# Performance work log

Measured on AMD Instinct MI355X. Metric: run time of the kernel, lower is better.

The kernel has to match this reference:

```python
import jax, jax.numpy as jnp
import numpy as np

B, DIM, H, W = 2, 192, 64, 64
HEADS = 4
EPS = 1e-12  # torch F.normalize eps


def conv2d(x, w, groups=1):
    # x: NCHW, w: OIHW, stride 1, SAME padding
    return jax.lax.conv_general_dilated(
        x, w, window_strides=(1, 1), padding='SAME',
        feature_group_count=groups,
        dimension_numbers=('NCHW', 'OIHW', 'NCHW'))


def setup_inputs() -> dict:
    key = jax.random.key(0)
    k1, k2, k3, k4 = jax.random.split(key, 4)
    x = jax.random.normal(k1, (B, DIM, H, W), dtype=jnp.float32)
    qkv_w = jax.random.normal(k2, (3 * DIM, DIM, 1, 1), dtype=jnp.float32) * 0.05
    dw_w = jax.random.normal(k3, (3 * DIM, 1, 3, 3), dtype=jnp.float32) * 0.05
    proj_w = jax.random.normal(k4, (DIM, DIM, 1, 1), dtype=jnp.float32) * 0.05
    temperature = jnp.ones((HEADS, 1, 1), dtype=jnp.float32)
    return {'x': x, 'qkv_w': qkv_w, 'dw_w': dw_w, 'proj_w': proj_w,
            'temperature': temperature}


def reference(x, qkv_w, dw_w, proj_w, temperature):
    b, dim, h, w = x.shape
    heads = temperature.shape[0]
    c = dim // heads  # per-head channels

    qkv = conv2d(conv2d(x, qkv_w), dw_w, groups=3 * dim)  # [b, 3*dim, h, w]
    q, k, v = jnp.split(qkv, 3, axis=1)

    def to_heads(t):
        # b (head c) h w -> b head (h w) c
        return t.reshape(b, heads, c, h * w).transpose(0, 1, 3, 2)

    q, k, v = to_heads(q), to_heads(k), to_heads(v)

    def l2norm(t):
        n = jnp.linalg.norm(t, axis=-1, keepdims=True)
        return t / jnp.maximum(n, EPS)

    q = l2norm(q)
    k = l2norm(k)

    # cosine attention with per-head learnable temperature
    attn = jnp.einsum('bnqc,bnkc->bnqk', q, k) * temperature[None]
    attn = jax.nn.softmax(attn, axis=-1)
    out = jnp.einsum('bnqk,bnkc->bnqc', attn, v)  # [b, head, hw, c]

    # b head (h w) c -> b (head c) h w
    out = out.transpose(0, 1, 3, 2).reshape(b, dim, h, w)
    return conv2d(out, proj_w)
```

## Files before the change

### kernel.cpp

```cpp
#include <hip/hip_runtime.h>
#include <cstdint>
#include <cstddef>

#define HW    4096
#define IMG   64
#define DIMC  192
#define NH    4
#define CH    48
#define CPAD  64
#define KVSPLIT 4
#define NTILE (HW / 64 / KVSPLIT)
#define LOG2E 1.4426950408889634f

typedef __bf16 bf16x8 __attribute__((ext_vector_type(8)));
typedef float  f32x4  __attribute__((ext_vector_type(4)));
typedef unsigned short u16x8 __attribute__((ext_vector_type(8)));

#if __has_builtin(__builtin_amdgcn_exp2f)
#define EXP2(x) __builtin_amdgcn_exp2f(x)
#else
#define EXP2(x) exp2f(x)
#endif

__device__ __forceinline__ unsigned short f2bf(float f) {
  unsigned int u = __builtin_bit_cast(unsigned int, f);
  u = (u + 0x7FFFu + ((u >> 16) & 1u)) >> 16;
  return (unsigned short)u;
}
__device__ __forceinline__ float bf2f(unsigned short u) {
  return __builtin_bit_cast(float, (unsigned int)u << 16);
}
__device__ __forceinline__ f32x4 mfma16(bf16x8 a, bf16x8 b, f32x4 c) {
  return __builtin_amdgcn_mfma_f32_16x16x32_bf16(a, b, c, 0, 0, 0);
}
__device__ __forceinline__ void gl16(const void* g, void* l) {
  __builtin_amdgcn_global_load_lds(
      (const __attribute__((address_space(1))) unsigned int*)g,
      (__attribute__((address_space(3))) unsigned int*)l, 16, 0, 0);
}

__global__ __launch_bounds__(256) void pack2_kernel(
    const float* __restrict__ x, const float* __restrict__ qkv_w,
    const float* __restrict__ proj_w, unsigned short* __restrict__ xb,
    unsigned short* __restrict__ wqkv, unsigned short* __restrict__ wproj) {
  const int bx = blockIdx.x, tid = threadIdx.x;
  if (bx < 64) {
    const int half = bx & 1;
    const int gpx = (bx >> 1) * 256 + tid;
    const int b = gpx >> 12, p = gpx & 4095;
    const int ch0 = half * 96;
    const float* src = x + ((size_t)b * DIMC + ch0) * HW + p;
    #pragma unroll
    for (int kc2 = 0; kc2 < 3; ++kc2) {
      const int kc = half * 3 + kc2;
      u16x8 g[4];
      #pragma unroll
      for (int v = 0; v < 4; ++v)
        #pragma unroll
        for (int j = 0; j < 8; ++j)
          g[v][j] = f2bf(src[(size_t)(kc2 * 32 + v * 8 + j) * HW]);
      unsigned short* dst = xb + (((size_t)b * 6 + kc) * HW + p) * 32;
      #pragma unroll
      for (int v = 0; v < 4; ++v) *(u16x8*)(dst + v * 8) = g[v];
    }
  } else {
    const int row = (bx - 64) * 256 + tid;
    if (row < 576) {
      const float* src = qkv_w + (size_t)row * DIMC;
      #pragma unroll
      for (int kc = 0; kc < 6; ++kc) {
        u16x8 g0, g1, g2, g3;
        #pragma unroll
        for (int j = 0; j < 8; ++j) {
          g0[j] = f2bf(src[kc * 32 + j]);      g1[j] = f2bf(src[kc * 32 + 8 + j]);
          g2[j] = f2bf(src[kc * 32 + 16 + j]); g3[j] = f2bf(src[kc * 32 + 24 + j]);
        }
        unsigned short* dst = wqkv + ((size_t)kc * 576 + row) * 32;
        *(u16x8*)dst = g0; *(u16x8*)(dst + 8) = g1;
        *(u16x8*)(dst + 16) = g2; *(u16x8*)(dst + 24) = g3;
      }
    } else {
      const int oc = row - 576;
      const float* src = proj_w + (size_t)oc * DIMC;
      #pragma unroll
      for (int kc = 0; kc < 6; ++kc) {
        u16x8 g0, g1, g2, g3;
        #pragma unroll
        for (int j = 0; j < 8; ++j) {
          g0[j] = f2bf(src[kc * 32 + j]);      g1[j] = f2bf(src[kc * 32 + 8 + j]);
          g2[j] = f2bf(src[kc * 32 + 16 + j]); g3[j] = f2bf(src[kc * 32 + 24 + j]);
        }
        unsigned short* dst = wproj + ((size_t)kc * DIMC + oc) * 32;
        *(u16x8*)dst = g0; *(u16x8*)(dst + 8) = g1;
        *(u16x8*)(dst + 16) = g2; *(u16x8*)(dst + 24) = g3;
      }
    }
  }
}

template <int PF, bool OBF>
__global__ __launch_bounds__(256) void wx_gemm2_kernel(
    const unsigned short* __restrict__ xb, const unsigned short* __restrict__ wb,
    void* __restrict__ Cout, int OC) {
  const int tid = threadIdx.x;
  const int lane = tid & 63, wv = tid >> 6;
  const int l15 = lane & 15, l4 = lane >> 4;
  const int oc0 = blockIdx.x * 64 + wv * 16;
  const int px0 = blockIdx.y * (PF * 16);
  const int b   = blockIdx.z;

  f32x4 acc[PF];
  #pragma unroll
  for (int p = 0; p < PF; ++p) acc[p] = f32x4{0.f, 0.f, 0.f, 0.f};

  #pragma unroll
  for (int kc = 0; kc < 6; ++kc) {
    const bf16x8 af = *(const bf16x8*)(wb + ((size_t)kc * OC + oc0 + l15) * 32 + l4 * 8);
    const unsigned short* xrow = xb + (((size_t)b * 6 + kc) * HW + px0 + l15) * 32 + l4 * 8;
    #pragma unroll
    for (int p = 0; p < PF; ++p) {
      const bf16x8 bf = *(const bf16x8*)(xrow + p * 512);
      acc[p] = mfma16(af, bf, acc[p]);
    }
  }
  if (OBF) {
    unsigned short* Cb = (unsigned short*)Cout + ((size_t)b * OC + oc0) * HW + px0;
    #pragma unroll
    for (int p = 0; p < PF; ++p)
      #pragma unroll
      for (int r = 0; r < 4; ++r)
        Cb[(size_t)(l4 * 4 + r) * HW + p * 16 + l15] = f2bf(acc[p][r]);
  } else {
    float* Cb = (float*)Cout + ((size_t)b * OC + oc0) * HW + px0;
    #pragma unroll
    for (int p = 0; p < PF; ++p)
      #pragma unroll
      for (int r = 0; r < 4; ++r)
        Cb[(size_t)(l4 * 4 + r) * HW + p * 16 + l15] = acc[p][r];
  }
}

__global__ __launch_bounds__(256) void dw_conv3_kernel(
    const unsigned short* __restrict__ X, const float* __restrict__ W,
    unsigned short* __restrict__ Y) {
  __shared__ float T[66][72];
  const int bc = blockIdx.x;
  const int ch = bc % 576;
  const int tid = threadIdx.x;
  const unsigned short* Xb = X + (size_t)bc * HW;
  #pragma unroll
  for (int i = 0; i < 4; ++i) {
    const int idx = i * 256 + tid;
    const int row = idx >> 4, c4 = (idx & 15) << 2;
    const ushort4 u = *(const ushort4*)(Xb + row * 64 + c4);
    float4 f; f.x = bf2f(u.x); f.y = bf2f(u.y); f.z = bf2f(u.z); f.w = bf2f(u.w);
    *(float4*)&T[row + 1][c4 + 4] = f;
  }
  if (tid < 72) { T[0][tid] = 0.f; T[65][tid] = 0.f; }
  if (tid >= 128 && tid < 194) { const int r = tid - 128; T[r][3] = 0.f; T[r][68] = 0.f; }
  float w[9];
  #pragma unroll
  for (int i = 0; i < 9; ++i) w[i] = W[ch * 9 + i];
  __syncthreads();

  const int xx = tid & 63, ys = (tid >> 6) << 4;
  const int c = xx + 4;
  float a0 = T[ys][c - 1],     a1 = T[ys][c],     a2 = T[ys][c + 1];
  float b0 = T[ys + 1][c - 1], b1 = T[ys + 1][c], b2 = T[ys + 1][c + 1];
  unsigned short* Yb = Y + (size_t)bc * HW;
  #pragma unroll
  for (int k = 0; k < 16; ++k) {
    const float c0 = T[ys + k + 2][c - 1], c1 = T[ys + k + 2][c], c2 = T[ys + k + 2][c + 1];
    const float s = w[0] * a0 + w[1] * a1 + w[2] * a2
                  + w[3] * b0 + w[4] * b1 + w[5] * b2
                  + w[6] * c0 + w[7] * c1 + w[8] * c2;
    Yb[(ys + k) * 64 + xx] = f2bf(s);
    a0 = b0; a1 = b1; a2 = b2; b0 = c0; b1 = c1; b2 = c2;
  }
}

__global__ __launch_bounds__(256) void norm_pack3_kernel(
    const unsigned short* __restrict__ Dw, const float* __restrict__ temp,
    unsigned short* __restrict__ Qr, unsigned short* __restrict__ Kr,
    unsigned short* __restrict__ Vs) {
  const int px = blockIdx.x * 256 + threadIdx.x;
  const int sel = blockIdx.y >> 2, h = blockIdx.y & 3;
  const int b = blockIdx.z;
  const int bh = b * NH + h;
  const unsigned short* base = Dw + ((size_t)b * 576 + sel * DIMC + h * CH) * HW + px;

  float v[CH];
  if (sel == 2) {
    const int kt = px & ~63, kl = px & 63;
    #pragma unroll
    for (int c = 0; c < CH; ++c)
      Vs[((size_t)bh * CH + c) * HW + kt + (kl ^ ((c & 7) << 3))] = base[(size_t)c * HW];
    return;
  }
  float ss = 0.f;
  #pragma unroll
  for (int j = 0; j < CH; ++j) { v[j] = bf2f(base[(size_t)j * HW]); ss += v[j] * v[j]; }
  const u16x8 zz = {0, 0, 0, 0, 0, 0, 0, 0};
  if (sel == 0) {
    const float sc = temp[h] * LOG2E / fmaxf(sqrtf(ss), 1e-12f);
    u16x8 gr[8];
    #pragma unroll
    for (int g = 0; g < 6; ++g)
      #pragma unroll
      for (int j = 0; j < 8; ++j) gr[g][j] = f2bf(v[g * 8 + j] * sc);
    gr[6] = zz; gr[7] = zz;
    unsigned short* qrow = Qr + ((size_t)bh * HW + px) * CPAD;
    #pragma unroll
    for (int g = 0; g < 8; ++g) *(u16x8*)(qrow + g * 8) = gr[g];
  } else {
    const int ksw = (px & 3) | (((px >> 3) & 1) << 2);
    const float sc = 1.0f / fmaxf(sqrtf(ss), 1e-12f);
    u16x8 gr[8];
    #pragma unroll
    for (int g = 0; g < 6; ++g)
      #pragma unroll
      for (int j = 0; j < 8; ++j) gr[g][j] = f2bf(v[g * 8 + j] * sc);
    gr[6] = zz; gr[7] = zz;
    unsigned short* krow = Kr + ((size_t)bh * HW + px) * CPAD;
    #pragma unroll
    for (int g = 0; g < 8; ++g) *(u16x8*)(krow + (g ^ ksw) * 8) = gr[g];
  }
}

__global__ __launch_bounds__(256, 2) void flash6_kernel(
    const unsigned short* __restrict__ Qr,
    const unsigned short* __restrict__ Kr,
    const unsigned short* __restrict__ Vs,
    const float* __restrict__ temp,
    unsigned short* __restrict__ Opart, float* __restrict__ Lpart) {
  __shared__ __align__(16) unsigned short Kl[2][64 * 64];
  __shared__ __align__(16) unsigned short Vl[2][64 * 64];
  const int tid = threadIdx.x;
  const int lane = tid & 63, wv = tid >> 6;
  const int l15 = lane & 15, l4 = lane >> 4;
  const int bh = blockIdx.x, qt = blockIdx.y, sp = blockIdx.z;
  const int qb = qt * 256 + wv * 64;
  const float m = fabsf(temp[bh & 3]) * LOG2E * 1.05f + 0.1f;

  for (int i = tid; i < 1024; i += 256) {
    const unsigned short vv = (i < 64) ? (unsigned short)0x3F80 : (unsigned short)0;
    Vl[0][3072 + i] = vv;
    Vl[1][3072 + i] = vv;
  }

  const unsigned short* Qb = Qr + ((size_t)bh * HW + qb) * CPAD;
  bf16x8 qf[4][2];
  #pragma unroll
  for (int qg = 0; qg < 4; ++qg)
    #pragma unroll
    for (int hh = 0; hh < 2; ++hh)
      qf[qg][hh] = *(const bf16x8*)(Qb + (size_t)(qg * 16 + l15) * CPAD + hh * 32 + l4 * 8);

  const char* kg = (const char*)Kr + ((size_t)bh * HW + (size_t)sp * (HW / KVSPLIT)) * 128;
  const char* vg = (const char*)Vs + (size_t)bh * CH * HW * 2 + (size_t)sp * (HW / KVSPLIT) * 2;
  const int koA = tid * 16;
  const int vgA = (tid >> 3) * 8192 + (tid & 7) * 16;
  const int vgB = (32 + (tid >> 3)) * 8192 + (tid & 7) * 16;

  auto stage = [&](int buf, const char* kp, const char* vp) {
    char* kl = (char*)&Kl[buf][0];
    gl16(kp + koA,        kl + koA);
    gl16(kp + 4096 + koA, kl + 4096 + koA);
    char* vl = (char*)&Vl[buf][0];
    gl16(vp + vgA, vl + tid * 16);
    if (tid < 128) gl16(vp + vgB, vl + 4096 + tid * 16);
  };

  f32x4 o[4][4];
  #pragma unroll
  for (int cg = 0; cg < 4; ++cg)
    #pragma unroll
    for (int qg = 0; qg < 4; ++qg) o[cg][qg] = f32x4{0.f, 0.f, 0.f, 0.f};
  const f32x4 zinit = {-m, -m, -m, -m};

  stage(0, kg, vg);
  kg += 8192; vg += 128;
  __syncthreads();
  int cur = 0;
  for (int t = 0; t < NTILE; ++t) {
    if (t + 1 < NTILE) { stage(cur ^ 1, kg, vg); kg += 8192; vg += 128; }
    const char* KL = (const char*)&Kl[cur][0];
    const char* VL = (const char*)&Vl[cur][0];

    f32x4 s[4][4];
    __builtin_amdgcn_s_setprio(1);
    #pragma unroll
    for (int n = 0; n < 4; ++n) {
      const int row = (n >> 1) * 32 + (l15 >> 2) * 8 + (n & 1) * 4 + (l15 & 3);
      const int sw = (l15 & 7) << 4;
      const bf16x8 kf0 = *(const bf16x8*)(KL + row * 128 + ((l4 << 4) ^ sw));
      const bf16x8 kf1 = *(const bf16x8*)(KL + row * 128 + (((4 + l4) << 4) ^ sw));
      #pragma unroll
      for (int qg = 0; qg < 4; ++qg) {
        f32x4 z = mfma16(kf0, qf[qg][0], zinit);
        s[qg][n] = mfma16(kf1, qf[qg][1], z);
      }
    }
    __builtin_amdgcn_s_setprio(0);

    #pragma unroll
    for (int qg = 0; qg < 4; ++qg)
      #pragma unroll
      for (int n = 0; n < 4; ++n)
        #pragma unroll
        for (int r = 0; r < 4; ++r)
          s[qg][n][r] = EXP2(s[qg][n][r]);

    #pragma unroll
    for (int kc = 0; kc < 2; ++kc) {
      bf16x8 pb[4];
      #pragma unroll
      for (int qg = 0; qg < 4; ++qg)
        #pragma unroll
        for (int j = 0; j < 8; ++j)
          pb[qg][j] = (__bf16)s[qg][kc * 2 + (j >> 2)][j & 3];
      __builtin_amdgcn_s_setprio(1);
      #pragma unroll
      for (int cg = 0; cg < 4; ++cg) {
        const int vrow = cg * 16 + l15;
        const bf16x8 vf = *(const bf16x8*)(VL + vrow * 128 + (((kc * 4 + l4) ^ (l15 & 7)) << 4));
        #pragma unroll
        for (int qg = 0; qg < 4; ++qg) o[cg][qg] = mfma16(vf, pb[qg], o[cg][qg]);
      }
      __builtin_amdgcn_s_setprio(0);
    }
    __syncthreads();
    cur ^= 1;
  }

  unsigned short* Ob = Opart + (size_t)(sp * 8 + bh) * CH * HW;
  #pragma unroll
  for (int cg = 0; cg < 3; ++cg)
    #pragma unroll
    for (int qg = 0; qg < 4; ++qg)
      #pragma unroll
      for (int r = 0; r < 4; ++r)
        Ob[(size_t)(cg * 16 + l4 * 4 + r) * HW + qb + qg * 16 + l15] = f2bf(o[cg][qg][r]);
  if (l4 == 0) {
    #pragma unroll
    for (int qg = 0; qg < 4; ++qg)
      Lpart[(size_t)(sp * 8 + bh) * HW + qb + qg * 16 + l15] = o[3][qg][0];
  }
}

__global__ __launch_bounds__(256) void combine3_kernel(
    const unsigned short* __restrict__ Opart, const float* __restrict__ Lpart,
    unsigned short* __restrict__ attnb) {
  const int tid = threadIdx.x;
  const int bh = blockIdx.x >> 5;
  const int q  = ((blockIdx.x & 31) << 7) + (tid & 127);
  const int half = tid >> 7;
  float lsum = 0.f;
  #pragma unroll
  for (int sp = 0; sp < KVSPLIT; ++sp) lsum += Lpart[(size_t)(sp * 8 + bh) * HW + q];
  const float inv = 1.f / lsum;
  const int b = bh >> 2, h = bh & 3;
  const int c0 = half * 24;
  float v[24];
  #pragma unroll
  for (int c = 0; c < 24; ++c) {
    float s = 0.f;
    #pragma unroll
    for (int sp = 0; sp < KVSPLIT; ++sp)
      s += bf2f(Opart[((size_t)(sp * 8 + bh) * CH + c0 + c) * HW + q]);
    v[c] = s * inv;
  }
  #pragma unroll
  for (int g = 0; g < 3; ++g) {
    const int ch0 = h * CH + c0 + g * 8;
    const int kc = ch0 >> 5, off = ch0 & 31;
    unsigned short* dst = attnb + (((size_t)b * 6 + kc) * HW + q) * 32 + off;
    u16x8 gg;
    #pragma unroll
    for (int j = 0; j < 8; ++j) gg[j] = f2bf(v[g * 8 + j]);
    *(u16x8*)dst = gg;
  }
}

extern "C" void kernel_launch(void* const* d_in, const int* in_sizes, int n_in,
                              void* d_out, int out_size, void* d_ws, size_t ws_size,
                              hipStream_t stream) {
  const float* x      = (const float*)d_in[0];
  const float* qkv_w  = (const float*)d_in[1];
  const float* dw_w   = (const float*)d_in[2];
  const float* proj_w = (const float*)d_in[3];
  const float* temp   = (const float*)d_in[4];

  char* ws = (char*)d_ws;
  unsigned short* xb    = (unsigned short*)(ws);
  unsigned short* wqkv  = (unsigned short*)(ws + 3145728);
  unsigned short* wproj = (unsigned short*)(ws + 3366912);
  unsigned short* qkvb  = (unsigned short*)(ws + 3440640);
  unsigned short* dwb   = (unsigned short*)(ws + 12877824);
  unsigned short* Qr    = (unsigned short*)(ws + 22315008);
  unsigned short* Kr    = (unsigned short*)(ws + 26509312);
  unsigned short* Vs    = (unsigned short*)(ws + 30703616);
  unsigned short* Opart = (unsigned short*)(ws + 33849344);
  float*          Lpart = (float*)(ws + 46432256);
  unsigned short* attnb = (unsigned short*)(ws + 46956544);

  pack2_kernel<<<dim3(67), 256, 0, stream>>>(x, qkv_w, proj_w, xb, wqkv, wproj);
  wx_gemm2_kernel<4, true><<<dim3(9, 64, 2), 256, 0, stream>>>(xb, wqkv, qkvb, 576);
  dw_conv3_kernel<<<dim3(1152), 256, 0, stream>>>(qkvb, dw_w, dwb);
  norm_pack3_kernel<<<dim3(16, 12, 2), 256, 0, stream>>>(dwb, temp, Qr, Kr, Vs);
  flash6_kernel<<<dim3(8, 16, KVSPLIT), 256, 0, stream>>>(Qr, Kr, Vs, temp, Opart, Lpart);
  combine3_kernel<<<dim3(256), 256, 0, stream>>>(Opart, Lpart, attnb);
  wx_gemm2_kernel<2, false><<<dim3(3, 128, 2), 256, 0, stream>>>(attnb, wproj, (float*)d_out, 192);
}
```

Measured before the change: 83.83 us.

## Use 32x32 MFMA in flash attention, fuse combine into projection GEMM

The attention kernel moves from 16x16x32 to 32x32x16 bf16 MFMA tiles and converts P to bf16 with packed converts plus a permlane32 swap. Its epilogue now goes through an LDS transpose so each query's output row is written contiguously. The split-KV combine kernel is removed and folded into the projection GEMM, which reduces the partials and normalises them while building its B operand. The QKV GEMM now reuses each activation fragment across three output-channel slices. Together these cut one launch and an intermediate buffer round trip, at the cost of fewer, heavier blocks in the GEMMs and more LDS and register pressure.

```diff
diff --git a/kernel.cpp b/kernel.cpp
--- a/kernel.cpp
+++ b/kernel.cpp
@@ -14,7 +14,9 @@
 
 typedef __bf16 bf16x8 __attribute__((ext_vector_type(8)));
 typedef float  f32x4  __attribute__((ext_vector_type(4)));
+typedef float  f32x16 __attribute__((ext_vector_type(16)));
 typedef unsigned short u16x8 __attribute__((ext_vector_type(8)));
+typedef unsigned int   u32x4 __attribute__((ext_vector_type(4)));
 
 #if __has_builtin(__builtin_amdgcn_exp2f)
 #define EXP2(x) __builtin_amdgcn_exp2f(x)
@@ -33,10 +35,21 @@
 __device__ __forceinline__ f32x4 mfma16(bf16x8 a, bf16x8 b, f32x4 c) {
   return __builtin_amdgcn_mfma_f32_16x16x32_bf16(a, b, c, 0, 0, 0);
 }
+__device__ __forceinline__ f32x16 mfma32(bf16x8 a, bf16x8 b, f32x16 c) {
+  return __builtin_amdgcn_mfma_f32_32x32x16_bf16(a, b, c, 0, 0, 0);
+}
 __device__ __forceinline__ void gl16(const void* g, void* l) {
   __builtin_amdgcn_global_load_lds(
       (const __attribute__((address_space(1))) unsigned int*)g,
       (__attribute__((address_space(3))) unsigned int*)l, 16, 0, 0);
+}
+__device__ __forceinline__ unsigned int cvtpk(float lo, float hi) {
+  unsigned int d;
+  asm("v_cvt_pk_bf16_f32 %0, %1, %2" : "=v"(d) : "v"(lo), "v"(hi));
+  return d;
+}
+__device__ __forceinline__ void swap32(unsigned int& a, unsigned int& b) {
+  asm("v_permlane32_swap_b32 %0, %1" : "+v"(a), "+v"(b));
 }
 
 __global__ __launch_bounds__(256) void pack2_kernel(
@@ -98,45 +111,44 @@
   }
 }
 
-template <int PF, bool OBF>
-__global__ __launch_bounds__(256) void wx_gemm2_kernel(
+__global__ __launch_bounds__(256) void qkv_gemm_kernel(
     const unsigned short* __restrict__ xb, const unsigned short* __restrict__ wb,
-    void* __restrict__ Cout, int OC) {
+    unsigned short* __restrict__ Cout) {
   const int tid = threadIdx.x;
   const int lane = tid & 63, wv = tid >> 6;
   const int l15 = lane & 15, l4 = lane >> 4;
-  const int oc0 = blockIdx.x * 64 + wv * 16;
-  const int px0 = blockIdx.y * (PF * 16);
+  const int ocbase = blockIdx.x * 192;
+  const int px0 = blockIdx.y * 64;
   const int b   = blockIdx.z;
 
-  f32x4 acc[PF];
-  #pragma unroll
-  for (int p = 0; p < PF; ++p) acc[p] = f32x4{0.f, 0.f, 0.f, 0.f};
+  f32x4 acc[3][4];
+  #pragma unroll
+  for (int s = 0; s < 3; ++s)
+    #pragma unroll
+    for (int p = 0; p < 4; ++p) acc[s][p] = f32x4{0.f, 0.f, 0.f, 0.f};
 
   #pragma unroll
   for (int kc = 0; kc < 6; ++kc) {
-    const bf16x8 af = *(const bf16x8*)(wb + ((size_t)kc * OC + oc0 + l15) * 32 + l4 * 8);
     const unsigned short* xrow = xb + (((size_t)b * 6 + kc) * HW + px0 + l15) * 32 + l4 * 8;
-    #pragma unroll
-    for (int p = 0; p < PF; ++p) {
-      const bf16x8 bf = *(const bf16x8*)(xrow + p * 512);
-      acc[p] = mfma16(af, bf, acc[p]);
-    }
-  }
-  if (OBF) {
-    unsigned short* Cb = (unsigned short*)Cout + ((size_t)b * OC + oc0) * HW + px0;
-    #pragma unroll
-    for (int p = 0; p < PF; ++p)
+    bf16x8 Bf[4];
+    #pragma unroll
+    for (int p = 0; p < 4; ++p) Bf[p] = *(const bf16x8*)(xrow + p * 512);
+    #pragma unroll
+    for (int s = 0; s < 3; ++s) {
+      const int oc = ocbase + s * 64 + wv * 16 + l15;
+      const bf16x8 af = *(const bf16x8*)(wb + ((size_t)kc * 576 + oc) * 32 + l4 * 8);
+      #pragma unroll
+      for (int p = 0; p < 4; ++p) acc[s][p] = mfma16(af, Bf[p], acc[s][p]);
+    }
+  }
+  #pragma unroll
+  for (int s = 0; s < 3; ++s) {
+    unsigned short* Cb = Cout + ((size_t)b * 576 + ocbase + s * 64 + wv * 16) * HW + px0;
+    #pragma unroll
+    for (int p = 0; p < 4; ++p)
       #pragma unroll
       for (int r = 0; r < 4; ++r)
-        Cb[(size_t)(l4 * 4 + r) * HW + p * 16 + l15] = f2bf(acc[p][r]);
-  } else {
-    float* Cb = (float*)Cout + ((size_t)b * OC + oc0) * HW + px0;
-    #pragma unroll
-    for (int p = 0; p < PF; ++p)
-      #pragma unroll
-      for (int r = 0; r < 4; ++r)
-        Cb[(size_t)(l4 * 4 + r) * HW + p * 16 + l15] = acc[p][r];
+        Cb[(size_t)(l4 * 4 + r) * HW + p * 16 + l15] = f2bf(acc[s][p][r]);
   }
 }
 
@@ -227,34 +239,36 @@
   }
 }
 
-__global__ __launch_bounds__(256, 2) void flash6_kernel(
+__global__ __launch_bounds__(256, 2) void flash7_kernel(
     const unsigned short* __restrict__ Qr,
     const unsigned short* __restrict__ Kr,
     const unsigned short* __restrict__ Vs,
     const float* __restrict__ temp,
     unsigned short* __restrict__ Opart, float* __restrict__ Lpart) {
-  __shared__ __align__(16) unsigned short Kl[2][64 * 64];
-  __shared__ __align__(16) unsigned short Vl[2][64 * 64];
+  __shared__ __align__(16) union {
+    struct { unsigned short Kl[2][4096]; unsigned short Vl[2][4096]; } s;
+    float T[256][53];
+  } lds;
   const int tid = threadIdx.x;
   const int lane = tid & 63, wv = tid >> 6;
-  const int l15 = lane & 15, l4 = lane >> 4;
+  const int l31 = lane & 31, lhi = lane >> 5;
   const int bh = blockIdx.x, qt = blockIdx.y, sp = blockIdx.z;
   const int qb = qt * 256 + wv * 64;
   const float m = fabsf(temp[bh & 3]) * LOG2E * 1.05f + 0.1f;
 
   for (int i = tid; i < 1024; i += 256) {
     const unsigned short vv = (i < 64) ? (unsigned short)0x3F80 : (unsigned short)0;
-    Vl[0][3072 + i] = vv;
-    Vl[1][3072 + i] = vv;
+    lds.s.Vl[0][3072 + i] = vv;
+    lds.s.Vl[1][3072 + i] = vv;
   }
 
   const unsigned short* Qb = Qr + ((size_t)bh * HW + qb) * CPAD;
-  bf16x8 qf[4][2];
-  #pragma unroll
-  for (int qg = 0; qg < 4; ++qg)
-    #pragma unroll
-    for (int hh = 0; hh < 2; ++hh)
-      qf[qg][hh] = *(const bf16x8*)(Qb + (size_t)(qg * 16 + l15) * CPAD + hh * 32 + l4 * 8);
+  bf16x8 qf[2][3];
+  #pragma unroll
+  for (int qb2 = 0; qb2 < 2; ++qb2)
+    #pragma unroll
+    for (int ci = 0; ci < 3; ++ci)
+      qf[qb2][ci] = *(const bf16x8*)(Qb + (size_t)(qb2 * 32 + l31) * CPAD + ci * 16 + lhi * 8);
 
   const char* kg = (const char*)Kr + ((size_t)bh * HW + (size_t)sp * (HW / KVSPLIT)) * 128;
   const char* vg = (const char*)Vs + (size_t)bh * CH * HW * 2 + (size_t)sp * (HW / KVSPLIT) * 2;
@@ -263,20 +277,24 @@
   const int vgB = (32 + (tid >> 3)) * 8192 + (tid & 7) * 16;
 
   auto stage = [&](int buf, const char* kp, const char* vp) {
-    char* kl = (char*)&Kl[buf][0];
+    char* kl = (char*)&lds.s.Kl[buf][0];
     gl16(kp + koA,        kl + koA);
     gl16(kp + 4096 + koA, kl + 4096 + koA);
-    char* vl = (char*)&Vl[buf][0];
+    char* vl = (char*)&lds.s.Vl[buf][0];
     gl16(vp + vgA, vl + tid * 16);
     if (tid < 128) gl16(vp + vgB, vl + 4096 + tid * 16);
   };
 
-  f32x4 o[4][4];
-  #pragma unroll
-  for (int cg = 0; cg < 4; ++cg)
-    #pragma unroll
-    for (int qg = 0; qg < 4; ++qg) o[cg][qg] = f32x4{0.f, 0.f, 0.f, 0.f};
-  const f32x4 zinit = {-m, -m, -m, -m};
+  f32x16 o[2][2];
+  #pragma unroll
+  for (int cb = 0; cb < 2; ++cb)
+    #pragma unroll
+    for (int qb2 = 0; qb2 < 2; ++qb2)
+      #pragma unroll
+      for (int i = 0; i < 16; ++i) o[cb][qb2][i] = 0.f;
+  f32x16 zin;
+  #pragma unroll
+  for (int i = 0; i < 16; ++i) zin[i] = -m;
 
   stage(0, kg, vg);
   kg += 8192; vg += 128;
@@ -284,48 +302,58 @@
   int cur = 0;
   for (int t = 0; t < NTILE; ++t) {
     if (t + 1 < NTILE) { stage(cur ^ 1, kg, vg); kg += 8192; vg += 128; }
-    const char* KL = (const char*)&Kl[cur][0];
-    const char* VL = (const char*)&Vl[cur][0];
-
-    f32x4 s[4][4];
+    const unsigned short* KL = &lds.s.Kl[cur][0];
+    const unsigned short* VL = &lds.s.Vl[cur][0];
+
+    f32x16 S[2][2];
     __builtin_amdgcn_s_setprio(1);
     #pragma unroll
-    for (int n = 0; n < 4; ++n) {
-      const int row = (n >> 1) * 32 + (l15 >> 2) * 8 + (n & 1) * 4 + (l15 & 3);
-      const int sw = (l15 & 7) << 4;
-      const bf16x8 kf0 = *(const bf16x8*)(KL + row * 128 + ((l4 << 4) ^ sw));
-      const bf16x8 kf1 = *(const bf16x8*)(KL + row * 128 + (((4 + l4) << 4) ^ sw));
-      #pragma unroll
-      for (int qg = 0; qg < 4; ++qg) {
-        f32x4 z = mfma16(kf0, qf[qg][0], zinit);
-        s[qg][n] = mfma16(kf1, qf[qg][1], z);
+    for (int kb = 0; kb < 2; ++kb) {
+      const int krow = kb * 32 + l31;
+      const int ksw = (krow & 3) | (((krow >> 3) & 1) << 2);
+      bf16x8 kf[3];
+      #pragma unroll
+      for (int ci = 0; ci < 3; ++ci)
+        kf[ci] = *(const bf16x8*)(KL + krow * 64 + (((ci * 2 + lhi) ^ ksw) * 8));
+      #pragma unroll
+      for (int qb2 = 0; qb2 < 2; ++qb2) {
+        f32x16 acc = zin;
+        #pragma unroll
+        for (int ci = 0; ci < 3; ++ci) acc = mfma32(kf[ci], qf[qb2][ci], acc);
+        S[kb][qb2] = acc;
       }
     }
     __builtin_amdgcn_s_setprio(0);
 
     #pragma unroll
-    for (int qg = 0; qg < 4; ++qg)
-      #pragma unroll
-      for (int n = 0; n < 4; ++n)
-        #pragma unroll
-        for (int r = 0; r < 4; ++r)
-          s[qg][n][r] = EXP2(s[qg][n][r]);
-
-    #pragma unroll
-    for (int kc = 0; kc < 2; ++kc) {
-      bf16x8 pb[4];
-      #pragma unroll
-      for (int qg = 0; qg < 4; ++qg)
-        #pragma unroll
-        for (int j = 0; j < 8; ++j)
-          pb[qg][j] = (__bf16)s[qg][kc * 2 + (j >> 2)][j & 3];
+    for (int kb = 0; kb < 2; ++kb)
+      #pragma unroll
+      for (int qb2 = 0; qb2 < 2; ++qb2)
+        #pragma unroll
+        for (int i = 0; i < 16; ++i) S[kb][qb2][i] = EXP2(S[kb][qb2][i]);
+
+    #pragma unroll
+    for (int kc = 0; kc < 4; ++kc) {
+      const int kb = kc >> 1, rb = (kc & 1) * 8;
+      bf16x8 pb[2];
+      #pragma unroll
+      for (int qb2 = 0; qb2 < 2; ++qb2) {
+        unsigned int w0 = cvtpk(S[kb][qb2][rb + 0], S[kb][qb2][rb + 1]);
+        unsigned int w1 = cvtpk(S[kb][qb2][rb + 2], S[kb][qb2][rb + 3]);
+        unsigned int w2 = cvtpk(S[kb][qb2][rb + 4], S[kb][qb2][rb + 5]);
+        unsigned int w3 = cvtpk(S[kb][qb2][rb + 6], S[kb][qb2][rb + 7]);
+        swap32(w0, w2);
+        swap32(w1, w3);
+        u32x4 ww = {w0, w1, w2, w3};
+        pb[qb2] = __builtin_bit_cast(bf16x8, ww);
+      }
       __builtin_amdgcn_s_setprio(1);
       #pragma unroll
-      for (int cg = 0; cg < 4; ++cg) {
-        const int vrow = cg * 16 + l15;
-        const bf16x8 vf = *(const bf16x8*)(VL + vrow * 128 + (((kc * 4 + l4) ^ (l15 & 7)) << 4));
-        #pragma unroll
-        for (int qg = 0; qg < 4; ++qg) o[cg][qg] = mfma16(vf, pb[qg], o[cg][qg]);
+      for (int cb = 0; cb < 2; ++cb) {
+        const int crow = cb * 32 + l31;
+        const bf16x8 vf = *(const bf16x8*)(VL + crow * 64 + (((kc * 2 + lhi) ^ (crow & 7)) * 8));
+        #pragma unroll
+        for (int qb2 = 0; qb2 < 2; ++qb2) o[cb][qb2] = mfma32(vf, pb[qb2], o[cb][qb2]);
       }
       __builtin_amdgcn_s_setprio(0);
     }
@@ -333,52 +361,92 @@
     cur ^= 1;
   }
 
-  unsigned short* Ob = Opart + (size_t)(sp * 8 + bh) * CH * HW;
-  #pragma unroll
-  for (int cg = 0; cg < 3; ++cg)
-    #pragma unroll
-    for (int qg = 0; qg < 4; ++qg)
+  #pragma unroll
+  for (int cb = 0; cb < 2; ++cb)
+    #pragma unroll
+    for (int qb2 = 0; qb2 < 2; ++qb2) {
+      const int ql = wv * 64 + qb2 * 32 + l31;
+      #pragma unroll
+      for (int r = 0; r < 16; ++r) {
+        const int c = cb * 32 + (r & 3) + 8 * (r >> 2) + 4 * lhi;
+        if (c < 48) lds.T[ql][c] = o[cb][qb2][r];
+      }
+      if (lhi == 0) lds.T[ql][48] = o[1][qb2][8];
+    }
+  __syncthreads();
+  {
+    const int ql = tid;
+    const int qg = qt * 256 + ql;
+    float vv[48];
+    #pragma unroll
+    for (int c = 0; c < 48; ++c) vv[c] = lds.T[ql][c];
+    const float L = lds.T[ql][48];
+    unsigned short* Ob = Opart + ((size_t)(sp * 8 + bh) * HW + qg) * 48;
+    #pragma unroll
+    for (int g = 0; g < 6; ++g) {
+      u16x8 gg;
+      #pragma unroll
+      for (int j = 0; j < 8; ++j) gg[j] = f2bf(vv[g * 8 + j]);
+      *(u16x8*)(Ob + g * 8) = gg;
+    }
+    Lpart[(size_t)(sp * 8 + bh) * HW + qg] = L;
+  }
+}
+
+__global__ __launch_bounds__(256) void proj_gemm_kernel(
+    const unsigned short* __restrict__ Opart, const float* __restrict__ Lpart,
+    const unsigned short* __restrict__ wb, float* __restrict__ Cout) {
+  const int tid = threadIdx.x;
+  const int lane = tid & 63, wv = tid >> 6;
+  const int l15 = lane & 15, l4 = lane >> 4;
+  const int px0 = blockIdx.y * 32;
+  const int b   = blockIdx.z;
+
+  bf16x8 Bf[6][2];
+  #pragma unroll
+  for (int kc = 0; kc < 6; ++kc) {
+    const int ch0 = kc * 32 + l4 * 8;
+    const int head = ch0 / 48, off = ch0 % 48;
+    #pragma unroll
+    for (int p = 0; p < 2; ++p) {
+      const int px = px0 + p * 16 + l15;
+      float ls = 0.f;
+      #pragma unroll
+      for (int sp = 0; sp < 4; ++sp)
+        ls += Lpart[(size_t)(sp * 8 + b * 4 + head) * HW + px];
+      const float inv = 1.f / ls;
+      float a8[8] = {};
+      #pragma unroll
+      for (int sp = 0; sp < 4; ++sp) {
+        const u16x8 u = *(const u16x8*)(Opart +
+            ((size_t)(sp * 8 + b * 4 + head) * HW + px) * 48 + off);
+        #pragma unroll
+        for (int j = 0; j < 8; ++j) a8[j] += bf2f(u[j]);
+      }
+      u16x8 g;
+      #pragma unroll
+      for (int j = 0; j < 8; ++j) g[j] = f2bf(a8[j] * inv);
+      Bf[kc][p] = __builtin_bit_cast(bf16x8, g);
+    }
+  }
+  #pragma unroll
+  for (int s = 0; s < 3; ++s) {
+    const int oc = s * 64 + wv * 16 + l15;
+    f32x4 acc[2];
+    #pragma unroll
+    for (int p = 0; p < 2; ++p) acc[p] = f32x4{0.f, 0.f, 0.f, 0.f};
+    #pragma unroll
+    for (int kc = 0; kc < 6; ++kc) {
+      const bf16x8 af = *(const bf16x8*)(wb + ((size_t)kc * DIMC + oc) * 32 + l4 * 8);
+      #pragma unroll
+      for (int p = 0; p < 2; ++p) acc[p] = mfma16(af, Bf[kc][p], acc[p]);
+    }
+    float* Cb = Cout + ((size_t)b * DIMC + s * 64 + wv * 16) * HW + px0;
+    #pragma unroll
+    for (int p = 0; p < 2; ++p)
       #pragma unroll
       for (int r = 0; r < 4; ++r)
-        Ob[(size_t)(cg * 16 + l4 * 4 + r) * HW + qb + qg * 16 + l15] = f2bf(o[cg][qg][r]);
-  if (l4 == 0) {
-    #pragma unroll
-    for (int qg = 0; qg < 4; ++qg)
-      Lpart[(size_t)(sp * 8 + bh) * HW + qb + qg * 16 + l15] = o[3][qg][0];
-  }
-}
-
-__global__ __launch_bounds__(256) void combine3_kernel(
-    const unsigned short* __restrict__ Opart, const float* __restrict__ Lpart,
-    unsigned short* __restrict__ attnb) {
-  const int tid = threadIdx.x;
-  const int bh = blockIdx.x >> 5;
-  const int q  = ((blockIdx.x & 31) << 7) + (tid & 127);
-  const int half = tid >> 7;
-  float lsum = 0.f;
-  #pragma unroll
-  for (int sp = 0; sp < KVSPLIT; ++sp) lsum += Lpart[(size_t)(sp * 8 + bh) * HW + q];
-  const float inv = 1.f / lsum;
-  const int b = bh >> 2, h = bh & 3;
-  const int c0 = half * 24;
-  float v[24];
-  #pragma unroll
-  for (int c = 0; c < 24; ++c) {
-    float s = 0.f;
-    #pragma unroll
-    for (int sp = 0; sp < KVSPLIT; ++sp)
-      s += bf2f(Opart[((size_t)(sp * 8 + bh) * CH + c0 + c) * HW + q]);
-    v[c] = s * inv;
-  }
-  #pragma unroll
-  for (int g = 0; g < 3; ++g) {
-    const int ch0 = h * CH + c0 + g * 8;
-    const int kc = ch0 >> 5, off = ch0 & 31;
-    unsigned short* dst = attnb + (((size_t)b * 6 + kc) * HW + q) * 32 + off;
-    u16x8 gg;
-    #pragma unroll
-    for (int j = 0; j < 8; ++j) gg[j] = f2bf(v[g * 8 + j]);
-    *(u16x8*)dst = gg;
+        Cb[(size_t)(l4 * 4 + r) * HW + p * 16 + l15] = acc[p][r];
   }
 }
 
@@ -402,13 +470,11 @@
   unsigned short* Vs    = (unsigned short*)(ws + 30703616);
   unsigned short* Opart = (unsigned short*)(ws + 33849344);
   float*          Lpart = (float*)(ws + 46432256);
-  unsigned short* attnb = (unsigned short*)(ws + 46956544);
 
   pack2_kernel<<<dim3(67), 256, 0, stream>>>(x, qkv_w, proj_w, xb, wqkv, wproj);
-  wx_gemm2_kernel<4, true><<<dim3(9, 64, 2), 256, 0, stream>>>(xb, wqkv, qkvb, 576);
+  qkv_gemm_kernel<<<dim3(3, 64, 2), 256, 0, stream>>>(xb, wqkv, qkvb);
   dw_conv3_kernel<<<dim3(1152), 256, 0, stream>>>(qkvb, dw_w, dwb);
   norm_pack3_kernel<<<dim3(16, 12, 2), 256, 0, stream>>>(dwb, temp, Qr, Kr, Vs);
-  flash6_kernel<<<dim3(8, 16, KVSPLIT), 256, 0, stream>>>(Qr, Kr, Vs, temp, Opart, Lpart);
-  combine3_kernel<<<dim3(256), 256, 0, stream>>>(Opart, Lpart, attnb);
-  wx_gemm2_kernel<2, false><<<dim3(3, 128, 2), 256, 0, stream>>>(attnb, wproj, (float*)d_out, 192);
-}
+  flash7_kernel<<<dim3(8, 16, KVSPLIT), 256, 0, stream>>>(Qr, Kr, Vs, temp, Opart, Lpart);
+  proj_gemm_kernel<<<dim3(1, 128, 2), 256, 0, stream>>>(Opart, Lpart, wproj, (float*)d_out);
+}
```

Measured after the change: 80.48 us. 1.04x faster.
